# Performance work log

Hardware: AMD Instinct MI355X
Metric: run time of the kernel (lower is better)

The kernel has to match this reference:

```python
import jax, jax.numpy as jnp
import numpy as np

N = 65536   # nodes
E = 262144  # edges
IN = 16     # input node feat dim
H0 = 16     # layer0 out dim
H1 = 8      # layer1 out dim (H0 // 2)
EA = 10     # edge attr dim (hardcoded in edge_nn)


def setup_inputs() -> dict:
    key = jax.random.key(0)
    ks = jax.random.split(key, 12)
    s = 0.05
    return {
        "x": jax.random.normal(ks[0], (N, IN), jnp.float32),
        "edge_index": jax.random.randint(ks[1], (2, E), 0, N),
        "edge_attr": jax.random.normal(ks[2], (E, EA), jnp.float32),
        # layer 0 edge MLP: Linear(10, 256) -> ReLU -> Linear(256, IN*H0)
        "w1_0": jax.random.normal(ks[3], (EA, H0 * H0), jnp.float32) * s,
        "b1_0": jnp.zeros((H0 * H0,), jnp.float32),
        "w2_0": jax.random.normal(ks[4], (H0 * H0, IN * H0), jnp.float32) * s,
        "b2_0": jnp.zeros((IN * H0,), jnp.float32),
        "root_0": jax.random.normal(ks[5], (IN, H0), jnp.float32) * s,
        "bias_0": jnp.zeros((H0,), jnp.float32),
        # layer 1 edge MLP: Linear(10, 256) -> ReLU -> Linear(256, H0*H1)
        "w1_1": jax.random.normal(ks[6], (EA, H0 * H0), jnp.float32) * s,
        "b1_1": jnp.zeros((H0 * H0,), jnp.float32),
        "w2_1": jax.random.normal(ks[7], (H0 * H0, H0 * H1), jnp.float32) * s,
        "b2_1": jnp.zeros((H0 * H1,), jnp.float32),
        "root_1": jax.random.normal(ks[8], (H0, H1), jnp.float32) * s,
        "bias_1": jnp.zeros((H1,), jnp.float32),
        # final edge classifier fc: Linear(2*H1, 1)
        "fc_w": jax.random.normal(ks[9], (2 * H1, 1), jnp.float32) * s,
        "fc_b": jnp.zeros((1,), jnp.float32),
    }


def _nnconv(x, src, dst, edge_attr, w1, b1, w2, b2, root, bias, in_c, out_c):
    # edge-conditioned weight generation: MLP(edge_attr) -> [E, in_c, out_c]
    h = jax.nn.relu(edge_attr @ w1 + b1)                 # [E, hid]
    We = (h @ w2 + b2).reshape(-1, in_c, out_c)          # [E, in, out]
    msg = jnp.einsum('ei,eio->eo', x[src], We)           # per-edge matmul [E, out]
    ssum = jax.ops.segment_sum(msg, dst, num_segments=N)               # [N, out]
    cnt = jax.ops.segment_sum(jnp.ones((msg.shape[0],), msg.dtype), dst, num_segments=N)
    agg = ssum / jnp.maximum(cnt, 1.0)[:, None]          # scatter-mean
    return agg + x @ root + bias                         # root transform + bias


def reference(x, edge_index, edge_attr, w1_0, b1_0, w2_0, b2_0, root_0, bias_0,
              w1_1, b1_1, w2_1, b2_1, root_1, bias_1, fc_w, fc_b):
    src, dst = edge_index[0], edge_index[1]
    # dropout is identity in eval mode
    x = jax.nn.relu(_nnconv(x, src, dst, edge_attr, w1_0, b1_0, w2_0, b2_0, root_0, bias_0, IN, H0))
    x = jax.nn.relu(_nnconv(x, src, dst, edge_attr, w1_1, b1_1, w2_1, b2_1, root_1, bias_1, H0, H1))
    ef = jnp.concatenate([x[src], x[dst]], axis=-1)      # [E, 2*H1]
    return jax.nn.sigmoid(ef @ fc_w + fc_b)              # [E, 1]
```

## Files before the change

### kernel.cpp

```cpp
#include <hip/hip_runtime.h>
#include <stdint.h>

#define NN 65536
#define NE 262144

typedef __attribute__((ext_vector_type(8))) short bf16x8;
typedef __attribute__((ext_vector_type(4))) float f32x4;

__device__ __forceinline__ short f2bf(float f) {
  union { float f; uint32_t u; } v; v.f = f;
  uint32_t u = v.u + 0x7fffu + ((v.u >> 16) & 1u);
  return (short)(u >> 16);
}
__device__ __forceinline__ float bf2f(short s) {
  union { uint32_t u; float f; } v; v.u = ((uint32_t)(uint16_t)s) << 16;
  return v.f;
}

__global__ __launch_bounds__(256) void prep_weights(
    const float* __restrict__ w1_0, const float* __restrict__ w1_1,
    const float* __restrict__ w2_0, const float* __restrict__ w2_1,
    short* __restrict__ w1t0, short* __restrict__ w1t1,
    short* __restrict__ w2t0, short* __restrict__ w2t1) {
  int t = blockIdx.x * 256 + threadIdx.x;
  if (t < 8192) {
    int n = t >> 5, k = t & 31;
    w1t0[t] = (k < 10) ? f2bf(w1_0[k * 256 + n]) : (short)0;
    w1t1[t] = (k < 10) ? f2bf(w1_1[k * 256 + n]) : (short)0;
  }
  if (t < 32768) {
    int n = t >> 8, k = t & 255;
    w2t1[t] = f2bf(w2_1[k * 128 + n]);
  }
  {
    int n = t >> 8, k = t & 255;
    w2t0[t] = f2bf(w2_0[k * 256 + n]);
  }
}

template <int N2, int OUTC, bool DO_CNT>
__global__ __launch_bounds__(256) void edge_kernel(
    const float* __restrict__ x, const int* __restrict__ ei,
    const float* __restrict__ ea, const short* __restrict__ w1t,
    const float* __restrict__ b1, const short* __restrict__ w2t,
    const float* __restrict__ b2, float* __restrict__ ssum,
    float* __restrict__ cnt) {
  __shared__ char smem[(64 * 32 + 64 * 256) * 2];
  char* const hB = smem + 64 * 32 * 2;
  short* const msgpre = (short*)smem;

  const int tid = threadIdx.x;
  const int wave = tid >> 6;
  const int lane = tid & 63;
  const int g = lane >> 4;
  const int lr = lane & 15;
  const int e0 = blockIdx.x * 64;

  for (int idx = tid; idx < 64 * 32; idx += 256) {
    int r = idx >> 5, k = idx & 31;
    float v = (k < 10) ? ea[(size_t)(e0 + r) * 10 + k] : 0.0f;
    *(short*)(smem + ((idx * 2) ^ ((r & 7) << 4))) = f2bf(v);
  }
  __syncthreads();

  f32x4 acc1[4][4];
#pragma unroll
  for (int mt = 0; mt < 4; ++mt)
#pragma unroll
    for (int nt = 0; nt < 4; ++nt) acc1[mt][nt] = (f32x4){0.f, 0.f, 0.f, 0.f};
  bf16x8 a1[4];
#pragma unroll
  for (int mt = 0; mt < 4; ++mt) {
    int row = mt * 16 + lr;
    a1[mt] = *(const bf16x8*)(smem + ((row * 64 + g * 16) ^ ((row & 7) << 4)));
  }
#pragma unroll
  for (int nt = 0; nt < 4; ++nt) {
    int col = wave * 64 + nt * 16 + lr;
    bf16x8 b = *(const bf16x8*)(w1t + col * 32 + g * 8);
#pragma unroll
    for (int mt = 0; mt < 4; ++mt)
      acc1[mt][nt] = __builtin_amdgcn_mfma_f32_16x16x32_bf16(a1[mt], b, acc1[mt][nt], 0, 0, 0);
  }
#pragma unroll
  for (int nt = 0; nt < 4; ++nt) {
    int col = wave * 64 + nt * 16 + lr;
    float bb = b1[col];
#pragma unroll
    for (int mt = 0; mt < 4; ++mt)
#pragma unroll
      for (int r = 0; r < 4; ++r) {
        int row = mt * 16 + g * 4 + r;
        float hv = fmaxf(acc1[mt][nt][r] + bb, 0.0f);
        *(short*)(hB + ((row * 512 + col * 2) ^ ((row & 7) << 4))) = f2bf(hv);
      }
  }
  __syncthreads();

  constexpr int NT2 = N2 / 64;
  f32x4 acc[4][NT2];
#pragma unroll
  for (int mt = 0; mt < 4; ++mt)
#pragma unroll
    for (int nt = 0; nt < NT2; ++nt) acc[mt][nt] = (f32x4){0.f, 0.f, 0.f, 0.f};
#pragma unroll
  for (int ks = 0; ks < 8; ++ks) {
    bf16x8 a2[4];
#pragma unroll
    for (int mt = 0; mt < 4; ++mt) {
      int row = mt * 16 + lr;
      a2[mt] = *(const bf16x8*)(hB + ((row * 512 + ks * 64 + g * 16) ^ ((row & 7) << 4)));
    }
#pragma unroll
    for (int nt = 0; nt < NT2; ++nt) {
      int col = wave * (NT2 * 16) + nt * 16 + lr;
      bf16x8 b = *(const bf16x8*)(w2t + col * 256 + ks * 32 + g * 8);
#pragma unroll
      for (int mt = 0; mt < 4; ++mt)
        acc[mt][nt] = __builtin_amdgcn_mfma_f32_16x16x32_bf16(a2[mt], b, acc[mt][nt], 0, 0, 0);
    }
  }
  __syncthreads();
#pragma unroll
  for (int nt = 0; nt < NT2; ++nt) {
    int col = wave * (NT2 * 16) + nt * 16 + lr;
    float bb = b2[col];
#pragma unroll
    for (int mt = 0; mt < 4; ++mt)
#pragma unroll
      for (int r = 0; r < 4; ++r) {
        int row = mt * 16 + g * 4 + r;
        msgpre[row * N2 + col] = f2bf(acc[mt][nt][r] + bb);
      }
  }
  __syncthreads();

  for (int it = tid; it < 64 * OUTC; it += 256) {
    int e = it / OUTC, o = it % OUTC;
    int ge = e0 + e;
    int s = ei[ge];
    int d = ei[NE + ge];
    const float* xr = x + (size_t)s * 16;
    float m = 0.f;
#pragma unroll
    for (int i = 0; i < 16; ++i)
      m += xr[i] * bf2f(msgpre[e * N2 + i * OUTC + o]);
    atomicAdd(&ssum[(size_t)d * OUTC + o], m);
    if (DO_CNT && o == 0) atomicAdd(&cnt[d], 1.0f);
  }
}

template <int OUTC>
__global__ __launch_bounds__(256) void node_kernel(
    const float* __restrict__ xin, const float* __restrict__ ssum,
    const float* __restrict__ cnt, const float* __restrict__ root,
    const float* __restrict__ bias, float* __restrict__ xout) {
  int n = blockIdx.x * 256 + threadIdx.x;
  float inv = 1.0f / fmaxf(cnt[n], 1.0f);
  float xi[16];
#pragma unroll
  for (int i = 0; i < 4; ++i) {
    float4 v = ((const float4*)(xin + (size_t)n * 16))[i];
    xi[4 * i] = v.x; xi[4 * i + 1] = v.y; xi[4 * i + 2] = v.z; xi[4 * i + 3] = v.w;
  }
#pragma unroll
  for (int o = 0; o < OUTC; ++o) {
    float a = ssum[(size_t)n * OUTC + o] * inv + bias[o];
#pragma unroll
    for (int i = 0; i < 16; ++i) a += xi[i] * root[i * OUTC + o];
    xout[(size_t)n * OUTC + o] = fmaxf(a, 0.f);
  }
}

__global__ __launch_bounds__(256) void final_kernel(
    const float* __restrict__ x2, const int* __restrict__ ei,
    const float* __restrict__ fcw, const float* __restrict__ fcb,
    float* __restrict__ out) {
  int e = blockIdx.x * 256 + threadIdx.x;
  int s = ei[e], d = ei[NE + e];
  float acc = fcb[0];
  const float* xs = x2 + (size_t)s * 8;
  const float* xd = x2 + (size_t)d * 8;
#pragma unroll
  for (int c = 0; c < 8; ++c) acc += xs[c] * fcw[c];
#pragma unroll
  for (int c = 0; c < 8; ++c) acc += xd[c] * fcw[8 + c];
  out[e] = 1.0f / (1.0f + __expf(-acc));
}

extern "C" void kernel_launch(void* const* d_in, const int* in_sizes, int n_in,
                              void* d_out, int out_size, void* d_ws, size_t ws_size,
                              hipStream_t stream) {
  const float* x      = (const float*)d_in[0];
  const int*   ei     = (const int*)d_in[1];
  const float* ea     = (const float*)d_in[2];
  const float* w1_0   = (const float*)d_in[3];
  const float* b1_0   = (const float*)d_in[4];
  const float* w2_0   = (const float*)d_in[5];
  const float* b2_0   = (const float*)d_in[6];
  const float* root_0 = (const float*)d_in[7];
  const float* bias_0 = (const float*)d_in[8];
  const float* w1_1   = (const float*)d_in[9];
  const float* b1_1   = (const float*)d_in[10];
  const float* w2_1   = (const float*)d_in[11];
  const float* b2_1   = (const float*)d_in[12];
  const float* root_1 = (const float*)d_in[13];
  const float* bias_1 = (const float*)d_in[14];
  const float* fc_w   = (const float*)d_in[15];
  const float* fc_b   = (const float*)d_in[16];
  float* out = (float*)d_out;

  char* ws = (char*)d_ws;
  float* ssum0 = (float*)(ws);
  float* x1    = (float*)(ws + (4u << 20));
  float* ssum1 = (float*)(ws + (8u << 20));
  float* x2    = (float*)(ws + (10u << 20));
  float* cnt   = (float*)(ws + (12u << 20));
  short* w1t0  = (short*)(ws + (12u << 20) + (256u << 10));
  short* w1t1  = w1t0 + 8192;
  short* w2t0  = w1t1 + 8192;
  short* w2t1  = w2t0 + 65536;

  hipMemsetAsync(ssum0, 0, (size_t)NN * 16 * 4, stream);
  hipMemsetAsync(ssum1, 0, (size_t)NN * 8 * 4, stream);
  hipMemsetAsync(cnt, 0, (size_t)NN * 4, stream);
  prep_weights<<<256, 256, 0, stream>>>(w1_0, w1_1, w2_0, w2_1, w1t0, w1t1, w2t0, w2t1);

  edge_kernel<256, 16, true><<<NE / 64, 256, 0, stream>>>(
      x, ei, ea, w1t0, b1_0, w2t0, b2_0, ssum0, cnt);
  node_kernel<16><<<NN / 256, 256, 0, stream>>>(x, ssum0, cnt, root_0, bias_0, x1);
  edge_kernel<128, 8, false><<<NE / 64, 256, 0, stream>>>(
      x1, ei, ea, w1t1, b1_1, w2t1, b2_1, ssum1, nullptr);
  node_kernel<8><<<NN / 256, 256, 0, stream>>>(x1, ssum1, cnt, root_1, bias_1, x2);
  final_kernel<<<NE / 256, 256, 0, stream>>>(x2, ei, fc_w, fc_b, out);
}
```

Measured before the change: 199.7 us.

## Fuse per-edge message contraction into MFMA epilogue and halve LDS footprint

The edge kernel now computes the hidden layer in two 128-column halves so the hidden buffer in LDS is half as large, and it sets launch bounds to allow three blocks per CU. The per-edge x[src]·We contraction is done directly on MFMA accumulator registers against gathered x rows staged in LDS, instead of writing a bf16 weight tensor to LDS and re-reading it. Partial sums are reduced across slots in LDS before the atomics. A separate prep pass converts edge attributes to padded bf16 once for both layers. This adds one kernel launch and an extra sync per half.

Result: slower. 290.1 us (+45.3%).

```diff
diff --git a/kernel.cpp b/kernel.cpp
--- a/kernel.cpp
+++ b/kernel.cpp
@@ -11,10 +11,6 @@
   union { float f; uint32_t u; } v; v.f = f;
   uint32_t u = v.u + 0x7fffu + ((v.u >> 16) & 1u);
   return (short)(u >> 16);
-}
-__device__ __forceinline__ float bf2f(short s) {
-  union { uint32_t u; float f; } v; v.u = ((uint32_t)(uint16_t)s) << 16;
-  return v.f;
 }
 
 __global__ __launch_bounds__(256) void prep_weights(
@@ -38,16 +34,30 @@
   }
 }
 
+__global__ __launch_bounds__(256) void prep_ea(const float* __restrict__ ea,
+                                               short* __restrict__ eab) {
+  int idx = blockIdx.x * 256 + threadIdx.x;
+  int e = idx >> 4, k = idx & 15;
+  eab[idx] = (k < 10) ? f2bf(ea[e * 10 + k]) : (short)0;
+}
+
 template <int N2, int OUTC, bool DO_CNT>
-__global__ __launch_bounds__(256) void edge_kernel(
+__global__ __launch_bounds__(256, 3) void edge_kernel(
     const float* __restrict__ x, const int* __restrict__ ei,
-    const float* __restrict__ ea, const short* __restrict__ w1t,
+    const short* __restrict__ eab, const short* __restrict__ w1t,
     const float* __restrict__ b1, const short* __restrict__ w2t,
     const float* __restrict__ b2, float* __restrict__ ssum,
     float* __restrict__ cnt) {
-  __shared__ char smem[(64 * 32 + 64 * 256) * 2];
-  char* const hB = smem + 64 * 32 * 2;
-  short* const msgpre = (short*)smem;
+  constexpr int NT2 = N2 / 64;
+  constexpr int LOGO = (OUTC == 16) ? 4 : 3;
+  constexpr int SLOTS = 4 * (16 / OUTC);
+  constexpr int PADO = OUTC + 1;
+  constexpr int PART = SLOTS * 64 * PADO * 4;
+  constexpr int HSZ = (PART > 64 * 128 * 2) ? PART : 64 * 128 * 2;
+  __shared__ alignas(16) char smem[HSZ + 64 * 20 * 4];
+  char* const hB = smem;
+  float* const partial = (float*)smem;
+  float* const xs = (float*)(smem + HSZ);
 
   const int tid = threadIdx.x;
   const int wave = tid >> 6;
@@ -56,98 +66,117 @@
   const int lr = lane & 15;
   const int e0 = blockIdx.x * 64;
 
-  for (int idx = tid; idx < 64 * 32; idx += 256) {
-    int r = idx >> 5, k = idx & 31;
-    float v = (k < 10) ? ea[(size_t)(e0 + r) * 10 + k] : 0.0f;
-    *(short*)(smem + ((idx * 2) ^ ((r & 7) << 4))) = f2bf(v);
-  }
-  __syncthreads();
-
-  f32x4 acc1[4][4];
-#pragma unroll
-  for (int mt = 0; mt < 4; ++mt)
-#pragma unroll
-    for (int nt = 0; nt < 4; ++nt) acc1[mt][nt] = (f32x4){0.f, 0.f, 0.f, 0.f};
+  {
+    int e = tid >> 2, q = tid & 3;
+    int s = ei[e0 + e];
+    float4 v = *(const float4*)(x + (size_t)s * 16 + q * 4);
+    *(float4*)(xs + e * 20 + q * 4) = v;
+  }
+
   bf16x8 a1[4];
 #pragma unroll
   for (int mt = 0; mt < 4; ++mt) {
     int row = mt * 16 + lr;
-    a1[mt] = *(const bf16x8*)(smem + ((row * 64 + g * 16) ^ ((row & 7) << 4)));
-  }
-#pragma unroll
-  for (int nt = 0; nt < 4; ++nt) {
-    int col = wave * 64 + nt * 16 + lr;
-    bf16x8 b = *(const bf16x8*)(w1t + col * 32 + g * 8);
+    if (g < 2)
+      a1[mt] = *(const bf16x8*)(eab + (size_t)(e0 + row) * 16 + g * 8);
+    else
+      a1[mt] = (bf16x8){0, 0, 0, 0, 0, 0, 0, 0};
+  }
+
+  f32x4 acc[4][NT2];
+#pragma unroll
+  for (int mt = 0; mt < 4; ++mt)
+#pragma unroll
+    for (int nt = 0; nt < NT2; ++nt) acc[mt][nt] = (f32x4){0.f, 0.f, 0.f, 0.f};
+
+#pragma unroll
+  for (int p = 0; p < 2; ++p) {
+    f32x4 acc1[4][2];
 #pragma unroll
     for (int mt = 0; mt < 4; ++mt)
-      acc1[mt][nt] = __builtin_amdgcn_mfma_f32_16x16x32_bf16(a1[mt], b, acc1[mt][nt], 0, 0, 0);
-  }
-#pragma unroll
-  for (int nt = 0; nt < 4; ++nt) {
-    int col = wave * 64 + nt * 16 + lr;
-    float bb = b1[col];
-#pragma unroll
-    for (int mt = 0; mt < 4; ++mt)
-#pragma unroll
-      for (int r = 0; r < 4; ++r) {
-        int row = mt * 16 + g * 4 + r;
-        float hv = fmaxf(acc1[mt][nt][r] + bb, 0.0f);
-        *(short*)(hB + ((row * 512 + col * 2) ^ ((row & 7) << 4))) = f2bf(hv);
+#pragma unroll
+      for (int n2 = 0; n2 < 2; ++n2) acc1[mt][n2] = (f32x4){0.f, 0.f, 0.f, 0.f};
+#pragma unroll
+    for (int n2 = 0; n2 < 2; ++n2) {
+      int colh = p * 128 + wave * 32 + n2 * 16 + lr;
+      bf16x8 b = *(const bf16x8*)(w1t + colh * 32 + g * 8);
+#pragma unroll
+      for (int mt = 0; mt < 4; ++mt)
+        acc1[mt][n2] = __builtin_amdgcn_mfma_f32_16x16x32_bf16(a1[mt], b, acc1[mt][n2], 0, 0, 0);
+    }
+#pragma unroll
+    for (int n2 = 0; n2 < 2; ++n2) {
+      int colh = p * 128 + wave * 32 + n2 * 16 + lr;
+      int c = wave * 32 + n2 * 16 + lr;
+      float bb = b1[colh];
+#pragma unroll
+      for (int mt = 0; mt < 4; ++mt)
+#pragma unroll
+        for (int r = 0; r < 4; ++r) {
+          int row = mt * 16 + g * 4 + r;
+          float hv = fmaxf(acc1[mt][n2][r] + bb, 0.0f);
+          *(short*)(hB + ((row * 256 + c * 2) ^ ((row & 7) << 4))) = f2bf(hv);
+        }
+    }
+    __syncthreads();
+#pragma unroll
+    for (int ks = 0; ks < 4; ++ks) {
+      bf16x8 a2[4];
+#pragma unroll
+      for (int mt = 0; mt < 4; ++mt) {
+        int row = mt * 16 + lr;
+        a2[mt] = *(const bf16x8*)(hB + ((row * 256 + ks * 64 + g * 16) ^ ((row & 7) << 4)));
       }
-  }
+#pragma unroll
+      for (int nt = 0; nt < NT2; ++nt) {
+        int colo = wave * (NT2 * 16) + nt * 16 + lr;
+        bf16x8 b = *(const bf16x8*)(w2t + colo * 256 + p * 128 + ks * 32 + g * 8);
+#pragma unroll
+        for (int mt = 0; mt < 4; ++mt)
+          acc[mt][nt] = __builtin_amdgcn_mfma_f32_16x16x32_bf16(a2[mt], b, acc[mt][nt], 0, 0, 0);
+      }
+    }
+    __syncthreads();
+  }
+
+  const int o = lr & (OUTC - 1);
+  const int slot = wave * (16 / OUTC) + (lr >> LOGO);
+  float b2c[NT2];
+  int iv[NT2];
+#pragma unroll
+  for (int nt = 0; nt < NT2; ++nt) {
+    int colo = wave * (NT2 * 16) + nt * 16 + lr;
+    b2c[nt] = b2[colo];
+    iv[nt] = colo >> LOGO;
+  }
+#pragma unroll
+  for (int mt = 0; mt < 4; ++mt)
+#pragma unroll
+    for (int r = 0; r < 4; ++r) {
+      int e = mt * 16 + g * 4 + r;
+      float m = 0.f;
+#pragma unroll
+      for (int nt = 0; nt < NT2; ++nt)
+        m += (acc[mt][nt][r] + b2c[nt]) * xs[e * 20 + iv[nt]];
+      partial[(slot * 64 + e) * PADO + o] = m;
+    }
   __syncthreads();
 
-  constexpr int NT2 = N2 / 64;
-  f32x4 acc[4][NT2];
-#pragma unroll
-  for (int mt = 0; mt < 4; ++mt)
-#pragma unroll
-    for (int nt = 0; nt < NT2; ++nt) acc[mt][nt] = (f32x4){0.f, 0.f, 0.f, 0.f};
-#pragma unroll
-  for (int ks = 0; ks < 8; ++ks) {
-    bf16x8 a2[4];
-#pragma unroll
-    for (int mt = 0; mt < 4; ++mt) {
-      int row = mt * 16 + lr;
-      a2[mt] = *(const bf16x8*)(hB + ((row * 512 + ks * 64 + g * 16) ^ ((row & 7) << 4)));
-    }
-#pragma unroll
-    for (int nt = 0; nt < NT2; ++nt) {
-      int col = wave * (NT2 * 16) + nt * 16 + lr;
-      bf16x8 b = *(const bf16x8*)(w2t + col * 256 + ks * 32 + g * 8);
-#pragma unroll
-      for (int mt = 0; mt < 4; ++mt)
-        acc[mt][nt] = __builtin_amdgcn_mfma_f32_16x16x32_bf16(a2[mt], b, acc[mt][nt], 0, 0, 0);
-    }
-  }
-  __syncthreads();
-#pragma unroll
-  for (int nt = 0; nt < NT2; ++nt) {
-    int col = wave * (NT2 * 16) + nt * 16 + lr;
-    float bb = b2[col];
-#pragma unroll
-    for (int mt = 0; mt < 4; ++mt)
-#pragma unroll
-      for (int r = 0; r < 4; ++r) {
-        int row = mt * 16 + g * 4 + r;
-        msgpre[row * N2 + col] = f2bf(acc[mt][nt][r] + bb);
-      }
-  }
-  __syncthreads();
-
-  for (int it = tid; it < 64 * OUTC; it += 256) {
-    int e = it / OUTC, o = it % OUTC;
-    int ge = e0 + e;
-    int s = ei[ge];
-    int d = ei[NE + ge];
-    const float* xr = x + (size_t)s * 16;
-    float m = 0.f;
-#pragma unroll
-    for (int i = 0; i < 16; ++i)
-      m += xr[i] * bf2f(msgpre[e * N2 + i * OUTC + o]);
-    atomicAdd(&ssum[(size_t)d * OUTC + o], m);
-    if (DO_CNT && o == 0) atomicAdd(&cnt[d], 1.0f);
-  }
+  constexpr int REP = 64 * OUTC / 256;
+  {
+    int e = tid >> 2;
+    int d = ei[NE + e0 + e];
+#pragma unroll
+    for (int j = 0; j < REP; ++j) {
+      int pr = tid * REP + j;
+      int oo = pr & (OUTC - 1);
+      float s = 0.f;
+#pragma unroll
+      for (int sl = 0; sl < SLOTS; ++sl) s += partial[(sl * 64 + e) * PADO + oo];
+      atomicAdd(&ssum[(size_t)d * OUTC + oo], s);
+    }
+  }
+  if (DO_CNT && tid < 64) atomicAdd(&cnt[ei[NE + e0 + tid]], 1.0f);
 }
 
 template <int OUTC>
@@ -179,12 +208,12 @@
   int e = blockIdx.x * 256 + threadIdx.x;
   int s = ei[e], d = ei[NE + e];
   float acc = fcb[0];
-  const float* xs = x2 + (size_t)s * 8;
-  const float* xd = x2 + (size_t)d * 8;
-#pragma unroll
-  for (int c = 0; c < 8; ++c) acc += xs[c] * fcw[c];
-#pragma unroll
-  for (int c = 0; c < 8; ++c) acc += xd[c] * fcw[8 + c];
+  const float* xsr = x2 + (size_t)s * 8;
+  const float* xdr = x2 + (size_t)d * 8;
+#pragma unroll
+  for (int c = 0; c < 8; ++c) acc += xsr[c] * fcw[c];
+#pragma unroll
+  for (int c = 0; c < 8; ++c) acc += xdr[c] * fcw[8 + c];
   out[e] = 1.0f / (1.0f + __expf(-acc));
 }
 
@@ -220,17 +249,19 @@
   short* w1t1  = w1t0 + 8192;
   short* w2t0  = w1t1 + 8192;
   short* w2t1  = w2t0 + 65536;
+  short* eab   = w2t1 + 32768;
 
   hipMemsetAsync(ssum0, 0, (size_t)NN * 16 * 4, stream);
   hipMemsetAsync(ssum1, 0, (size_t)NN * 8 * 4, stream);
   hipMemsetAsync(cnt, 0, (size_t)NN * 4, stream);
   prep_weights<<<256, 256, 0, stream>>>(w1_0, w1_1, w2_0, w2_1, w1t0, w1t1, w2t0, w2t1);
+  prep_ea<<<NE * 16 / 256, 256, 0, stream>>>(ea, eab);
 
   edge_kernel<256, 16, true><<<NE / 64, 256, 0, stream>>>(
-      x, ei, ea, w1t0, b1_0, w2t0, b2_0, ssum0, cnt);
+      x, ei, eab, w1t0, b1_0, w2t0, b2_0, ssum0, cnt);
   node_kernel<16><<<NN / 256, 256, 0, stream>>>(x, ssum0, cnt, root_0, bias_0, x1);
   edge_kernel<128, 8, false><<<NE / 64, 256, 0, stream>>>(
-      x1, ei, ea, w1t1, b1_1, w2t1, b2_1, ssum1, nullptr);
+      x1, ei, eab, w1t1, b1_1, w2t1, b2_1, ssum1, nullptr);
   node_kernel<8><<<NN / 256, 256, 0, stream>>>(x1, ssum1, cnt, root_1, bias_1, x2);
   final_kernel<<<NE / 256, 256, 0, stream>>>(x2, ei, fc_w, fc_b, out);
 }
```
